# Kernel tuning notes

Measured on AMD Instinct MI355X. Metric: run time of the kernel, lower is better.

The kernel has to match this reference:

```python
import jax, jax.numpy as jnp
import numpy as np

TQ, TV, TA = 40, 64, 40
B = 2048
D = 1280          # per-stream feature dim; 4*D == 10*EMBED
EMBED = 512
EPS = 1e-5


def setup_inputs() -> dict:
    key = jax.random.key(0)
    ks = jax.random.split(key, 10)
    q  = jax.random.normal(ks[0], (TQ, B, D), jnp.float32)
    vq = jax.random.normal(ks[1], (TV, B, D), jnp.float32)
    a  = jax.random.normal(ks[2], (TA, B, D), jnp.float32)
    va = jax.random.normal(ks[3], (TV, B, D), jnp.float32)
    qlen = jax.random.randint(ks[4], (B,), 1, TQ + 1, dtype=jnp.int32)
    alen = jax.random.randint(ks[5], (B,), 1, TA + 1, dtype=jnp.int32)
    # classifier params (xavier-ish init)
    W1 = jax.random.normal(ks[6], (4 * D, EMBED), jnp.float32) * (2.0 / (4 * D + EMBED)) ** 0.5
    b1 = jnp.zeros((EMBED,), jnp.float32)
    gamma = jnp.ones((EMBED,), jnp.float32)
    beta = jnp.zeros((EMBED,), jnp.float32)
    W2 = jax.random.normal(ks[7], (EMBED, 1), jnp.float32) * (2.0 / (EMBED + 1)) ** 0.5
    b2 = jnp.zeros((1,), jnp.float32)
    return dict(question_embedding_v=q, visual_embedding_qu=vq,
                answer_embedding_v_expand=a, visual_embedding_an_expand=va,
                W1=W1, b1=b1, gamma=gamma, beta=beta, W2=W2, b2=b2,
                question_len=qlen, answers_len=alen)


def _masked_mean(x, lens):
    # x: [T, B, D], lens: [B] -> mean over first lens[j] timesteps per sample -> [B, D]
    T = x.shape[0]
    mask = (jnp.arange(T)[:, None] < lens[None, :]).astype(x.dtype)  # [T, B]
    return jnp.einsum('tbd,tb->bd', x, mask) / lens.astype(x.dtype)[:, None]


def reference(question_embedding_v, visual_embedding_qu,
              answer_embedding_v_expand, visual_embedding_an_expand,
              W1, b1, gamma, beta, W2, b2,
              question_len, answers_len):
    q  = _masked_mean(question_embedding_v, question_len)          # [B, D]
    vq = visual_embedding_qu.mean(axis=0)                          # [B, D]
    a  = _masked_mean(answer_embedding_v_expand, answers_len)      # [B, D]
    va = visual_embedding_an_expand.mean(axis=0)                   # [B, D]
    feat = jnp.concatenate([q, vq, a, va], axis=1)                 # [B, 4D] = [B, 10*EMBED]
    # Dropout is identity in eval/reference; BatchNorm1d uses batch stats (training mode).
    h = jax.nn.elu(feat @ W1 + b1)                                 # [B, EMBED]
    mu = h.mean(axis=0)
    var = h.var(axis=0)                                            # biased, like torch BN
    h = (h - mu) * jax.lax.rsqrt(var + EPS) * gamma + beta
    return h @ W2 + b2                                             # [B, 1]
```

## Files before the change

kernel.cpp:

```cpp
#include <hip/hip_runtime.h>
#include <hip/hip_bf16.h>

typedef __attribute__((ext_vector_type(8))) short bf16x8;
typedef __attribute__((ext_vector_type(4))) float f32x4;

#define NB 2048
#define ND 1280
#define NK 5120
#define NE 512

static __device__ inline unsigned short f2bf(float x) {
    union { float f; unsigned u; } c; c.f = x;
    unsigned r = c.u + 0x7FFFu + ((c.u >> 16) & 1u);
    return (unsigned short)(r >> 16);
}

__global__ __launch_bounds__(256) void reduce_w1t_kernel(
    const f32x4* __restrict__ q, const f32x4* __restrict__ vq,
    const f32x4* __restrict__ aa, const f32x4* __restrict__ va,
    const int* __restrict__ qlen, const int* __restrict__ alen,
    ushort4* __restrict__ feat,
    const float* __restrict__ W1, unsigned short* __restrict__ w1t,
    float* __restrict__ s1s2)
{
    __shared__ unsigned short lds[32][33];

    if (blockIdx.x >= 5120) {
        const int bid = blockIdx.x - 5120;
        if (bid == 0) {
            ((f32x4*)s1s2)[threadIdx.x] = (f32x4){0.f, 0.f, 0.f, 0.f};
        }
        const int kb = (bid >> 4) * 32;
        const int nb = (bid & 15) * 32;
        const int tx = threadIdx.x & 31;
        const int ty = threadIdx.x >> 5;
        #pragma unroll
        for (int i = 0; i < 4; ++i) {
            int k = kb + ty + i * 8;
            lds[ty + i * 8][tx] = f2bf(W1[(long)k * NE + nb + tx]);
        }
        __syncthreads();
        #pragma unroll
        for (int i = 0; i < 4; ++i) {
            int n = nb + ty + i * 8;
            w1t[(long)n * NK + kb + tx] = lds[tx][ty + i * 8];
        }
        return;
    }

    const int tid = blockIdx.x * 256 + threadIdx.x;
    const int per_seg = NB * 160;
    const int seg = tid / per_seg;
    const int r = tid - seg * per_seg;
    const int b = r / 160;
    const int ch = r - b * 160;

    const long base = (long)b * 320 + ch;
    const long stride = (long)NB * 320;

    f32x4 a0 = {0.f, 0.f, 0.f, 0.f};
    f32x4 a1 = {0.f, 0.f, 0.f, 0.f};
    float inv;

    if (seg == 1 || seg == 3) {
        const f32x4* src = (seg == 1) ? vq : va;
        #pragma unroll 8
        for (int t = 0; t < 64; ++t) {
            f32x4 v0 = __builtin_nontemporal_load(&src[base + (long)t * stride]);
            f32x4 v1 = __builtin_nontemporal_load(&src[base + 160 + (long)t * stride]);
            a0 += v0;
            a1 += v1;
        }
        inv = 1.0f / 64.0f;
    } else {
        const f32x4* src = (seg == 0) ? q : aa;
        const int len = (seg == 0) ? qlen[b] : alen[b];
        #pragma unroll 4
        for (int t = 0; t < len; ++t) {
            f32x4 v0 = __builtin_nontemporal_load(&src[base + (long)t * stride]);
            f32x4 v1 = __builtin_nontemporal_load(&src[base + 160 + (long)t * stride]);
            a0 += v0;
            a1 += v1;
        }
        inv = 1.0f / (float)len;
    }

    ushort4 o0, o1;
    o0.x = f2bf(a0.x * inv); o0.y = f2bf(a0.y * inv);
    o0.z = f2bf(a0.z * inv); o0.w = f2bf(a0.w * inv);
    o1.x = f2bf(a1.x * inv); o1.y = f2bf(a1.y * inv);
    o1.z = f2bf(a1.z * inv); o1.w = f2bf(a1.w * inv);
    const long fb = (long)b * (NK / 4) + seg * 320 + ch;
    feat[fb] = o0;
    feat[fb + 160] = o1;
}

__global__ __launch_bounds__(256) void gemm_kernel(
    const unsigned short* __restrict__ feat, const unsigned short* __restrict__ w1t,
    const float* __restrict__ b1,
    float* __restrict__ h, float* __restrict__ s1s2)
{
    __shared__ int4 As[32 * 9];
    __shared__ int4 Bs[64 * 9];

    const int bid = blockIdx.x;
    const int m0 = (bid >> 3) << 5;
    const int n0 = (bid & 7) << 6;

    const int t = threadIdx.x;
    const int l = t & 63;
    const int w = t >> 6;
    const int wm = (w >> 1) << 4;
    const int wn = (w & 1) << 5;
    const int srow = t >> 3;
    const int scol = t & 7;

    f32x4 acc[2] = {};

    for (int k0 = 0; k0 < NK; k0 += 64) {
        int4 av = *(const int4*)(feat + (long)(m0 + srow) * NK + k0 + scol * 8);
        int4 b0v = *(const int4*)(w1t + (long)(n0 + srow) * NK + k0 + scol * 8);
        int4 b1v = *(const int4*)(w1t + (long)(n0 + 32 + srow) * NK + k0 + scol * 8);
        As[srow * 9 + scol] = av;
        Bs[srow * 9 + scol] = b0v;
        Bs[(srow + 32) * 9 + scol] = b1v;
        __syncthreads();
        #pragma unroll
        for (int kk = 0; kk < 2; ++kk) {
            const int kc = kk * 4 + (l >> 4);
            bf16x8 af = *(const bf16x8*)&As[(wm + (l & 15)) * 9 + kc];
            bf16x8 bf0 = *(const bf16x8*)&Bs[(wn + (l & 15)) * 9 + kc];
            bf16x8 bf1 = *(const bf16x8*)&Bs[(wn + 16 + (l & 15)) * 9 + kc];
            acc[0] = __builtin_amdgcn_mfma_f32_16x16x32_bf16(af, bf0, acc[0], 0, 0, 0);
            acc[1] = __builtin_amdgcn_mfma_f32_16x16x32_bf16(af, bf1, acc[1], 0, 0, 0);
        }
        __syncthreads();
    }

    const int rbase = m0 + wm + ((l >> 4) << 2);
    #pragma unroll
    for (int ni = 0; ni < 2; ++ni) {
        const int col = n0 + wn + ni * 16 + (l & 15);
        const float bias = b1[col];
        float s1 = 0.f, s2 = 0.f;
        #pragma unroll
        for (int rr = 0; rr < 4; ++rr) {
            float v = acc[ni][rr] + bias;
            v = v > 0.f ? v : expm1f(v);
            h[(long)(rbase + rr) * NE + col] = v;
            s1 += v; s2 += v * v;
        }
        s1 += __shfl_xor(s1, 16); s2 += __shfl_xor(s2, 16);
        s1 += __shfl_xor(s1, 32); s2 += __shfl_xor(s2, 32);
        if (l < 16) {
            unsafeAtomicAdd(&s1s2[col], s1);
            unsafeAtomicAdd(&s1s2[NE + col], s2);
        }
    }
}

__global__ __launch_bounds__(256) void out_kernel(
    const float* __restrict__ h, const float* __restrict__ s1s2,
    const float* __restrict__ gamma, const float* __restrict__ beta,
    const float* __restrict__ W2, const float* __restrict__ b2,
    float* __restrict__ out)
{
    __shared__ float coef[NE];
    __shared__ float red[256];
    const int t = threadIdx.x;

    float term = 0.f;
    #pragma unroll
    for (int i = 0; i < 2; ++i) {
        const int e = t + i * 256;
        const float s1 = s1s2[e];
        const float s2 = s1s2[NE + e];
        const float mu = s1 * (1.0f / NB);
        const float var = s2 * (1.0f / NB) - mu * mu;
        const float rs = rsqrtf(var + 1e-5f);
        const float g = gamma[e], wv = W2[e];
        coef[e] = rs * g * wv;
        term += (beta[e] - mu * rs * g) * wv;
    }
    red[t] = term;
    __syncthreads();
    #pragma unroll
    for (int off = 128; off > 0; off >>= 1) {
        if (t < off) red[t] += red[t + off];
        __syncthreads();
    }
    const float cst = red[0] + b2[0];

    const int w = t >> 6;
    const int l = t & 63;
    const int row = blockIdx.x * 4 + w;
    const f32x4* h4 = (const f32x4*)(h + (long)row * NE);
    f32x4 x0 = h4[l * 2], x1 = h4[l * 2 + 1];
    f32x4 c0 = *(const f32x4*)&coef[l * 8];
    f32x4 c1 = *(const f32x4*)&coef[l * 8 + 4];
    float dot = x0.x * c0.x + x0.y * c0.y + x0.z * c0.z + x0.w * c0.w
              + x1.x * c1.x + x1.y * c1.y + x1.z * c1.z + x1.w * c1.w;
    #pragma unroll
    for (int off = 32; off > 0; off >>= 1) dot += __shfl_down(dot, off);
    if (l == 0) out[row] = dot + cst;
}

extern "C" void kernel_launch(void* const* d_in, const int* in_sizes, int n_in,
                              void* d_out, int out_size, void* d_ws, size_t ws_size,
                              hipStream_t stream)
{
    const float* q    = (const float*)d_in[0];
    const float* vq   = (const float*)d_in[1];
    const float* aa   = (const float*)d_in[2];
    const float* va   = (const float*)d_in[3];
    const float* W1   = (const float*)d_in[4];
    const float* b1   = (const float*)d_in[5];
    const float* gam  = (const float*)d_in[6];
    const float* bet  = (const float*)d_in[7];
    const float* W2   = (const float*)d_in[8];
    const float* b2   = (const float*)d_in[9];
    const int* qlen   = (const int*)d_in[10];
    const int* alen   = (const int*)d_in[11];
    float* out = (float*)d_out;

    char* ws = (char*)d_ws;
    unsigned short* feat = (unsigned short*)ws;
    unsigned short* w1t  = (unsigned short*)(ws + 20971520);
    float* hbuf          = (float*)(ws + 26214400);
    float* s1s2          = (float*)(ws + 30408704);

    reduce_w1t_kernel<<<7680, 256, 0, stream>>>(
        (const f32x4*)q, (const f32x4*)vq, (const f32x4*)aa, (const f32x4*)va,
        qlen, alen, (ushort4*)feat, W1, w1t, s1s2);

    gemm_kernel<<<512, 256, 0, stream>>>(feat, w1t, b1, hbuf, s1s2);

    out_kernel<<<512, 256, 0, stream>>>(hbuf, s1s2, gam, bet, W2, b2, out);
}
```

Baseline: 375.6 us.

## Enlarge GEMM tile to 64x64 with register prefetch and reorder reduce segments

The GEMM block tile grows from 32x64 to 64x64, so each wave computes a 2x2 set of MFMA tiles. The next K-slice is prefetched into registers while the current one is computed, and the grid is halved to 256 blocks. The reduce kernel now schedules the full-length visual segments first and the variable-length masked segments last, and unrolls the masked loop further. Each block reuses more data per load, at the cost of fewer blocks to occupy the CUs during the GEMM.

```diff
diff --git a/kernel.cpp b/kernel.cpp
--- a/kernel.cpp
+++ b/kernel.cpp
@@ -48,10 +48,11 @@
         return;
     }
 
-    const int tid = blockIdx.x * 256 + threadIdx.x;
-    const int per_seg = NB * 160;
-    const int seg = tid / per_seg;
-    const int r = tid - seg * per_seg;
+    const int sb = blockIdx.x / 1280;
+    const int rem = blockIdx.x - sb * 1280;
+    const int seg = (sb == 0) ? 1 : (sb == 1) ? 3 : (sb == 2) ? 0 : 2;
+
+    const int r = rem * 256 + threadIdx.x;
     const int b = r / 160;
     const int ch = r - b * 160;
 
@@ -75,7 +76,7 @@
     } else {
         const f32x4* src = (seg == 0) ? q : aa;
         const int len = (seg == 0) ? qlen[b] : alen[b];
-        #pragma unroll 4
+        #pragma unroll 8
         for (int t = 0; t < len; ++t) {
             f32x4 v0 = __builtin_nontemporal_load(&src[base + (long)t * stride]);
             f32x4 v1 = __builtin_nontemporal_load(&src[base + 160 + (long)t * stride]);
@@ -100,55 +101,73 @@
     const float* __restrict__ b1,
     float* __restrict__ h, float* __restrict__ s1s2)
 {
-    __shared__ int4 As[32 * 9];
+    __shared__ int4 As[64 * 9];
     __shared__ int4 Bs[64 * 9];
 
     const int bid = blockIdx.x;
-    const int m0 = (bid >> 3) << 5;
+    const int m0 = (bid >> 3) << 6;
     const int n0 = (bid & 7) << 6;
 
     const int t = threadIdx.x;
     const int l = t & 63;
     const int w = t >> 6;
-    const int wm = (w >> 1) << 4;
+    const int wm = (w >> 1) << 5;
     const int wn = (w & 1) << 5;
-    const int srow = t >> 3;
-    const int scol = t & 7;
-
-    f32x4 acc[2] = {};
+    const int srow = t >> 2;
+    const int sc = (t & 3) << 1;
+
+    const unsigned short* Ab = feat + (long)(m0 + srow) * NK + sc * 8;
+    const unsigned short* Bb = w1t + (long)(n0 + srow) * NK + sc * 8;
+
+    f32x4 acc[2][2] = {};
+
+    int4 a0 = *(const int4*)(Ab);
+    int4 a1 = *(const int4*)(Ab + 8);
+    int4 b0 = *(const int4*)(Bb);
+    int4 b1v = *(const int4*)(Bb + 8);
 
     for (int k0 = 0; k0 < NK; k0 += 64) {
-        int4 av = *(const int4*)(feat + (long)(m0 + srow) * NK + k0 + scol * 8);
-        int4 b0v = *(const int4*)(w1t + (long)(n0 + srow) * NK + k0 + scol * 8);
-        int4 b1v = *(const int4*)(w1t + (long)(n0 + 32 + srow) * NK + k0 + scol * 8);
-        As[srow * 9 + scol] = av;
-        Bs[srow * 9 + scol] = b0v;
-        Bs[(srow + 32) * 9 + scol] = b1v;
-        __syncthreads();
+        As[srow * 9 + sc] = a0;
+        As[srow * 9 + sc + 1] = a1;
+        Bs[srow * 9 + sc] = b0;
+        Bs[srow * 9 + sc + 1] = b1v;
+        __syncthreads();
+        if (k0 + 64 < NK) {
+            a0 = *(const int4*)(Ab + k0 + 64);
+            a1 = *(const int4*)(Ab + k0 + 72);
+            b0 = *(const int4*)(Bb + k0 + 64);
+            b1v = *(const int4*)(Bb + k0 + 72);
+        }
         #pragma unroll
         for (int kk = 0; kk < 2; ++kk) {
             const int kc = kk * 4 + (l >> 4);
-            bf16x8 af = *(const bf16x8*)&As[(wm + (l & 15)) * 9 + kc];
+            bf16x8 af0 = *(const bf16x8*)&As[(wm + (l & 15)) * 9 + kc];
+            bf16x8 af1 = *(const bf16x8*)&As[(wm + 16 + (l & 15)) * 9 + kc];
             bf16x8 bf0 = *(const bf16x8*)&Bs[(wn + (l & 15)) * 9 + kc];
             bf16x8 bf1 = *(const bf16x8*)&Bs[(wn + 16 + (l & 15)) * 9 + kc];
-            acc[0] = __builtin_amdgcn_mfma_f32_16x16x32_bf16(af, bf0, acc[0], 0, 0, 0);
-            acc[1] = __builtin_amdgcn_mfma_f32_16x16x32_bf16(af, bf1, acc[1], 0, 0, 0);
-        }
-        __syncthreads();
-    }
-
-    const int rbase = m0 + wm + ((l >> 4) << 2);
+            acc[0][0] = __builtin_amdgcn_mfma_f32_16x16x32_bf16(af0, bf0, acc[0][0], 0, 0, 0);
+            acc[0][1] = __builtin_amdgcn_mfma_f32_16x16x32_bf16(af0, bf1, acc[0][1], 0, 0, 0);
+            acc[1][0] = __builtin_amdgcn_mfma_f32_16x16x32_bf16(af1, bf0, acc[1][0], 0, 0, 0);
+            acc[1][1] = __builtin_amdgcn_mfma_f32_16x16x32_bf16(af1, bf1, acc[1][1], 0, 0, 0);
+        }
+        __syncthreads();
+    }
+
+    const int r0 = m0 + wm + ((l >> 4) << 2);
     #pragma unroll
     for (int ni = 0; ni < 2; ++ni) {
         const int col = n0 + wn + ni * 16 + (l & 15);
         const float bias = b1[col];
         float s1 = 0.f, s2 = 0.f;
         #pragma unroll
-        for (int rr = 0; rr < 4; ++rr) {
-            float v = acc[ni][rr] + bias;
-            v = v > 0.f ? v : expm1f(v);
-            h[(long)(rbase + rr) * NE + col] = v;
-            s1 += v; s2 += v * v;
+        for (int mi = 0; mi < 2; ++mi) {
+            #pragma unroll
+            for (int rr = 0; rr < 4; ++rr) {
+                float v = acc[mi][ni][rr] + bias;
+                v = v > 0.f ? v : expm1f(v);
+                h[(long)(r0 + mi * 16 + rr) * NE + col] = v;
+                s1 += v; s2 += v * v;
+            }
         }
         s1 += __shfl_xor(s1, 16); s2 += __shfl_xor(s2, 16);
         s1 += __shfl_xor(s1, 32); s2 += __shfl_xor(s2, 32);
@@ -233,7 +252,7 @@
         (const f32x4*)q, (const f32x4*)vq, (const f32x4*)aa, (const f32x4*)va,
         qlen, alen, (ushort4*)feat, W1, w1t, s1s2);
 
-    gemm_kernel<<<512, 256, 0, stream>>>(feat, w1t, b1, hbuf, s1s2);
+    gemm_kernel<<<256, 256, 0, stream>>>(feat, w1t, b1, hbuf, s1s2);
 
     out_kernel<<<512, 256, 0, stream>>>(hbuf, s1s2, gam, bet, W2, b2, out);
 }
```

After: 355.6 us. -5.3%, faster.
